# Optimization experiments

Hardware: AMD Instinct MI355X
Metric: run time of the kernel (lower is better)

The kernel has to match this reference:

```python
import jax, jax.numpy as jnp
import numpy as np

D, H, DH, L, F, NM = 512, 8, 64, 8, 2048, 80
B, S = 8, 1024


def _ln(x, g, b, eps=1e-5):
    mu = x.mean(-1, keepdims=True)
    var = ((x - mu) ** 2).mean(-1, keepdims=True)
    return (x - mu) / jnp.sqrt(var + eps) * g + b


def setup_inputs() -> dict:
    key = jax.random.key(0)
    ks = jax.random.split(key, 16)
    n = lambda k, sh: jax.random.normal(k, sh, dtype=jnp.float32) * 0.02
    # sinusoidal positional encoding, as in PositionalEncoding
    pos = np.arange(S, dtype=np.float32)[:, None]
    div = np.exp(np.arange(0, D, 2, dtype=np.float32) * (-np.log(10000.0) / D))
    pe = np.zeros((S, D), dtype=np.float32)
    pe[:, 0::2] = np.sin(pos * div)
    pe[:, 1::2] = np.cos(pos * div)
    return dict(
        mel=jax.random.normal(ks[0], (B, S, NM), dtype=jnp.float32),
        pe=jnp.asarray(pe),
        proj_w=n(ks[1], (NM, D)), proj_b=jnp.zeros((D,), jnp.float32),
        Wq=n(ks[2], (L, D, D)), bq=jnp.zeros((L, D), jnp.float32),
        Wk=n(ks[3], (L, D, D)), bk=jnp.zeros((L, D), jnp.float32),
        Wv=n(ks[4], (L, D, D)), bv=jnp.zeros((L, D), jnp.float32),
        Wo=n(ks[5], (L, D, D)), bo=jnp.zeros((L, D), jnp.float32),
        ln1_g=jnp.ones((L, D), jnp.float32), ln1_b=jnp.zeros((L, D), jnp.float32),
        ln2_g=jnp.ones((L, D), jnp.float32), ln2_b=jnp.zeros((L, D), jnp.float32),
        Wi=n(ks[6], (L, D, F)), bi=jnp.zeros((L, F), jnp.float32),
        Wf=n(ks[7], (L, F, D)), bf=jnp.zeros((L, D), jnp.float32),
        lnf_g=jnp.ones((D,), jnp.float32), lnf_b=jnp.zeros((D,), jnp.float32),
        lang_w=n(ks[8], (D, 100)), lang_b=jnp.zeros((100,), jnp.float32),
        int_w=n(ks[9], (D, 50)), int_b=jnp.zeros((50,), jnp.float32),
        emo_w=n(ks[10], (D, 8)), emo_b=jnp.zeros((8,), jnp.float32),
        sp_w=n(ks[11], (D, 1000)), sp_b=jnp.zeros((1000,), jnp.float32),
    )


def reference(mel, pe, proj_w, proj_b, Wq, bq, Wk, bk, Wv, bv, Wo, bo,
              ln1_g, ln1_b, ln2_g, ln2_b, Wi, bi, Wf, bf,
              lnf_g, lnf_b, lang_w, lang_b, int_w, int_b, emo_w, emo_b, sp_w, sp_b):
    # feature extraction projection + positional encoding
    h = mel @ proj_w + proj_b + pe[None]  # (B, S, D)
    scale = 1.0 / np.sqrt(DH)

    def block(h, p):
        wq, bq_, wk, bk_, wv, bv_, wo, bo_, g1, b1, g2, b2, wi, bi_, wf, bf_ = p
        x = _ln(h, g1, b1)
        b, s, _ = x.shape
        heads = lambda y, w, bias: (y @ w + bias).reshape(b, s, H, DH).transpose(0, 2, 1, 3)
        q, k, v = heads(x, wq, bq_), heads(x, wk, bk_), heads(x, wv, bv_)
        probs = jax.nn.softmax(jnp.einsum('bhqd,bhkd->bhqk', q, k) * scale, axis=-1)
        ctx = jnp.einsum('bhqk,bhkd->bhqd', probs, v).transpose(0, 2, 1, 3).reshape(b, s, D)
        h = h + ctx @ wo + bo_
        y = _ln(h, g2, b2)
        h = h + jax.nn.gelu(y @ wi + bi_, approximate=False) @ wf + bf_
        return h, None

    h, _ = jax.lax.scan(block, h, (Wq, bq, Wk, bk, Wv, bv, Wo, bo,
                                   ln1_g, ln1_b, ln2_g, ln2_b, Wi, bi, Wf, bf))
    h = _ln(h, lnf_g, lnf_b)
    pooled = h.mean(axis=1)  # no mask: sequence_lengths=None path
    language_logits = pooled @ lang_w + lang_b
    intent_logits = pooled @ int_w + int_b
    emotion_logits = pooled @ emo_w + emo_b
    speech_logits = h @ sp_w + sp_b
    return (language_logits, intent_logits, emotion_logits, speech_logits)
```

## Files before the change

### kernel.cpp

```cpp
#include <hip/hip_runtime.h>
#include <hip/hip_bf16.h>
#include <math.h>

#define DD   512
#define HH   8
#define DHH  64
#define LL   8
#define FF   2048
#define NMEL 80
#define BB   8
#define SS   1024
#define MM   (BB*SS)

typedef __attribute__((ext_vector_type(8))) short bf16x8;
typedef __attribute__((ext_vector_type(4))) float f32x4;
typedef __attribute__((ext_vector_type(4))) unsigned short u16x4;
typedef __attribute__((ext_vector_type(8))) unsigned short u16x8;

#define GLOAD_LDS16(g, l) __builtin_amdgcn_global_load_lds( \
    (const __attribute__((address_space(1))) void*)(g),      \
    (__attribute__((address_space(3))) void*)(l), 16, 0, 0)

__device__ __forceinline__ unsigned short f2bf(float x) {
    __hip_bfloat16 b = __float2bfloat16(x);
    return *reinterpret_cast<unsigned short*>(&b);
}

__global__ __launch_bounds__(256) void proj_pe_kernel(
    const float* __restrict__ mel, const float* __restrict__ pw,
    const float* __restrict__ pb, const float* __restrict__ pe,
    float* __restrict__ h)
{
    int row = blockIdx.x;
    int s = row & (SS - 1);
    __shared__ float m_s[NMEL];
    int t = threadIdx.x;
    if (t < NMEL) m_s[t] = mel[(size_t)row * NMEL + t];
    __syncthreads();
    for (int d = t; d < DD; d += 256) {
        float acc = pb[d] + pe[(size_t)s * DD + d];
        #pragma unroll 8
        for (int k = 0; k < NMEL; ++k)
            acc = fmaf(m_s[k], pw[(size_t)k * DD + d], acc);
        h[(size_t)row * DD + d] = acc;
    }
}

__global__ __launch_bounds__(512) void ln_kernel(
    const float* __restrict__ in, const float* __restrict__ g,
    const float* __restrict__ bta, __hip_bfloat16* __restrict__ out)
{
    int w = threadIdx.x >> 6, lane = threadIdx.x & 63;
    int row = blockIdx.x * 8 + w;
    const float4* xr = reinterpret_cast<const float4*>(in + (size_t)row * DD) + lane * 2;
    float4 v0 = xr[0], v1 = xr[1];
    float s  = v0.x + v0.y + v0.z + v0.w + v1.x + v1.y + v1.z + v1.w;
    float ss = v0.x*v0.x + v0.y*v0.y + v0.z*v0.z + v0.w*v0.w
             + v1.x*v1.x + v1.y*v1.y + v1.z*v1.z + v1.w*v1.w;
    #pragma unroll
    for (int off = 1; off < 64; off <<= 1) {
        s  += __shfl_xor(s, off);
        ss += __shfl_xor(ss, off);
    }
    float mu  = s * (1.f / DD);
    float var = ss * (1.f / DD) - mu * mu;
    float rstd = rsqrtf(var + 1e-5f);
    const float4* gp = reinterpret_cast<const float4*>(g) + lane * 2;
    const float4* bp = reinterpret_cast<const float4*>(bta) + lane * 2;
    float4 g0 = gp[0], g1 = gp[1], b0 = bp[0], b1 = bp[1];
    u16x8 o;
    o[0] = f2bf((v0.x - mu) * rstd * g0.x + b0.x);
    o[1] = f2bf((v0.y - mu) * rstd * g0.y + b0.y);
    o[2] = f2bf((v0.z - mu) * rstd * g0.z + b0.z);
    o[3] = f2bf((v0.w - mu) * rstd * g0.w + b0.w);
    o[4] = f2bf((v1.x - mu) * rstd * g1.x + b1.x);
    o[5] = f2bf((v1.y - mu) * rstd * g1.y + b1.y);
    o[6] = f2bf((v1.z - mu) * rstd * g1.z + b1.z);
    o[7] = f2bf((v1.w - mu) * rstd * g1.w + b1.w);
    *reinterpret_cast<u16x8*>(out + (size_t)row * DD + lane * 8) = o;
}

__global__ __launch_bounds__(256) void wconv_kernel(
    const float* __restrict__ in, __hip_bfloat16* __restrict__ out,
    int K, int N, int rstride, int rowoff)
{
    __shared__ float tile[32][33];
    size_t lin  = (size_t)blockIdx.z * K * N;
    size_t lout = (size_t)blockIdx.z * rstride * K + (size_t)rowoff * K;
    int tx = threadIdx.x & 31, ty = threadIdx.x >> 5;
    int n0 = blockIdx.x * 32, k0 = blockIdx.y * 32;
    #pragma unroll
    for (int i = 0; i < 32; i += 8) {
        int k = k0 + ty + i, n = n0 + tx;
        tile[ty + i][tx] = (n < N) ? in[lin + (size_t)k * N + n] : 0.f;
    }
    __syncthreads();
    #pragma unroll
    for (int i = 0; i < 32; i += 8) {
        int n = n0 + ty + i, k = k0 + tx;
        out[lout + (size_t)n * K + k] = __float2bfloat16(tile[tx][ty + i]);
    }
}

template<int OUTMODE, bool GELU_EP, bool RESID>
__global__ __launch_bounds__(512) void gemm_bf16(
    const __hip_bfloat16* __restrict__ A,
    const __hip_bfloat16* __restrict__ Bt,
    const float* __restrict__ b0, const float* __restrict__ b1,
    const float* __restrict__ b2,
    const float* __restrict__ resid,
    float* __restrict__ Cf,
    __hip_bfloat16* __restrict__ O0, __hip_bfloat16* __restrict__ O1,
    __hip_bfloat16* __restrict__ O2,
    int M, int N, int K)
{
    __shared__ __align__(16) __hip_bfloat16 As[128 * 64];
    __shared__ __align__(16) __hip_bfloat16 Bs[128 * 64];
    int t = threadIdx.x;
    int w = t >> 6, lane = t & 63, g = lane >> 4, li = lane & 15;
    int wm = w >> 2, wn = w & 3;

    int nwg = gridDim.x * gridDim.y;
    int lin = blockIdx.y * gridDim.x + blockIdx.x;
    int xcd = lin & 7, idx = lin >> 3;
    int q8 = nwg >> 3, r8 = nwg & 7;
    int swz = (xcd < r8 ? xcd * (q8 + 1) : r8 * (q8 + 1) + (xcd - r8) * q8) + idx;
    size_t bm = (size_t)(swz / gridDim.x) * 128;
    size_t bn = (size_t)(swz % gridDim.x) * 128;

    const f32x4 vzero = {0.f, 0.f, 0.f, 0.f};
    f32x4 acc[4][2];
    #pragma unroll
    for (int i = 0; i < 4; ++i)
        #pragma unroll
        for (int j = 0; j < 2; ++j) acc[i][j] = vzero;

    for (int k0 = 0; k0 < K; k0 += 64) {
        #pragma unroll
        for (int i = 0; i < 2; ++i) {
            int c = i * 512 + t;
            int row = c >> 3, col = (c & 7) << 3;
            GLOAD_LDS16(A + (bm + row) * (size_t)K + k0 + col, As + (size_t)c * 8);
        }
        #pragma unroll
        for (int i = 0; i < 2; ++i) {
            int c = i * 512 + t;
            int row = c >> 3, col = (c & 7) << 3;
            GLOAD_LDS16(Bt + (bn + row) * (size_t)K + k0 + col, Bs + (size_t)c * 8);
        }
        __syncthreads();
        #pragma unroll
        for (int kk = 0; kk < 2; ++kk) {
            bf16x8 af[4], bfr[2];
            #pragma unroll
            for (int mi = 0; mi < 4; ++mi)
                af[mi] = *reinterpret_cast<const bf16x8*>(As + (wm * 64 + mi * 16 + li) * 64 + kk * 32 + g * 8);
            #pragma unroll
            for (int ni = 0; ni < 2; ++ni)
                bfr[ni] = *reinterpret_cast<const bf16x8*>(Bs + (wn * 32 + ni * 16 + li) * 64 + kk * 32 + g * 8);
            #pragma unroll
            for (int mi = 0; mi < 4; ++mi)
                #pragma unroll
                for (int ni = 0; ni < 2; ++ni)
                    acc[mi][ni] = __builtin_amdgcn_mfma_f32_16x16x32_bf16(af[mi], bfr[ni], acc[mi][ni], 0, 0, 0);
        }
        __syncthreads();
    }

    #pragma unroll
    for (int mi = 0; mi < 4; ++mi) {
        #pragma unroll
        for (int ni = 0; ni < 2; ++ni) {
            f32x4 v = acc[mi][ni];
            int coll = wn * 32 + ni * 16 + li;
            size_t col = bn + coll;
            if ((int)col >= N) continue;
            float bv;
            int sel = 0, c = (int)col;
            if (OUTMODE == 2) {
                sel = (int)(col >> 9); c = (int)(col & 511);
                bv = (sel == 0) ? b0[c] : (sel == 1) ? b1[c] : b2[c];
            } else {
                bv = b0[col];
            }
            #pragma unroll
            for (int r = 0; r < 4; ++r) {
                size_t row = bm + wm * 64 + mi * 16 + g * 4 + r;
                float x = v[r] + bv;
                if (GELU_EP) x = 0.5f * x * (1.f + erff(x * 0.70710678118654752440f));
                if (RESID)   x += resid[row * (size_t)N + col];
                if (OUTMODE == 0) {
                    Cf[row * (size_t)N + col] = x;
                } else if (OUTMODE == 1) {
                    O0[row * (size_t)N + col] = __float2bfloat16(x);
                } else {
                    size_t b = row >> 10, s = row & (SS - 1);
                    size_t h = (size_t)(c >> 6), d = (size_t)(c & 63);
                    __hip_bfloat16 xb = __float2bfloat16(x);
                    if (sel == 0)      O0[((b * HH + h) << 16) + (s << 6) + d] = xb;
                    else if (sel == 1) O1[((b * HH + h) << 16) + (s << 6) + d] = xb;
                    else               O2[((b * HH + h) << 16) + (d << 10) + s] = xb;
                }
            }
        }
    }
}

__global__ __launch_bounds__(512, 4) void attn_mfma(
    const __hip_bfloat16* __restrict__ qb,
    const __hip_bfloat16* __restrict__ kb,
    const __hip_bfloat16* __restrict__ vtb,
    __hip_bfloat16* __restrict__ ctx)
{
    __shared__ __align__(16) char smem[49152];
    unsigned short (*Plds)[32][40] = (unsigned short (*)[32][40])smem;
    float* comb = (float*)smem;

    int t = threadIdx.x;
    int w = t >> 6, lane = t & 63, g = lane >> 4, li = lane & 15;
    int wq = w & 3, wk = w >> 2;
    int bh = blockIdx.x;
    int b = bh >> 3, h = bh & 7;
    int q0 = blockIdx.y * 128 + wq * 32;

    const __hip_bfloat16* Qp = qb  + ((size_t)bh << 16);
    const __hip_bfloat16* Kp = kb  + ((size_t)bh << 16);
    const __hip_bfloat16* Vp = vtb + ((size_t)bh << 16);

    bf16x8 qf[2][2];
    #pragma unroll
    for (int qt = 0; qt < 2; ++qt)
        #pragma unroll
        for (int kk = 0; kk < 2; ++kk)
            qf[qt][kk] = *reinterpret_cast<const bf16x8*>(
                Qp + (size_t)(q0 + qt * 16 + li) * DHH + kk * 32 + g * 8);

    const f32x4 vzero = {0.f, 0.f, 0.f, 0.f};
    f32x4 acc_oT[2][4];
    float m_r[2], l_r[2];
    #pragma unroll
    for (int qt = 0; qt < 2; ++qt) {
        #pragma unroll
        for (int dt = 0; dt < 4; ++dt) acc_oT[qt][dt] = vzero;
        m_r[qt] = -1e30f; l_r[qt] = 0.f;
    }

    const float csc = 0.125f * 1.44269504088896340736f;

    for (int it = 0; it < 16; ++it) {
        int ks0 = wk * 512 + it * 32;
        f32x4 accs[2][2];
        #pragma unroll
        for (int qt = 0; qt < 2; ++qt)
            #pragma unroll
            for (int kt = 0; kt < 2; ++kt) accs[qt][kt] = vzero;
        #pragma unroll
        for (int kk = 0; kk < 2; ++kk) {
            bf16x8 kf[2];
            #pragma unroll
            for (int kt = 0; kt < 2; ++kt)
                kf[kt] = *reinterpret_cast<const bf16x8*>(
                    Kp + (size_t)(ks0 + kt * 16 + li) * DHH + kk * 32 + g * 8);
            #pragma unroll
            for (int qt = 0; qt < 2; ++qt)
                #pragma unroll
                for (int kt = 0; kt < 2; ++kt)
                    accs[qt][kt] = __builtin_amdgcn_mfma_f32_16x16x32_bf16(kf[kt], qf[qt][kk], accs[qt][kt], 0, 0, 0);
        }

        float mnew[2];
        #pragma unroll
        for (int qt = 0; qt < 2; ++qt) {
            float a0 = fmaxf(fmaxf(accs[qt][0][0], accs[qt][0][1]),
                             fmaxf(accs[qt][0][2], accs[qt][0][3]));
            float a1 = fmaxf(fmaxf(accs[qt][1][0], accs[qt][1][1]),
                             fmaxf(accs[qt][1][2], accs[qt][1][3]));
            float m = fmaxf(a0, a1);
            m = fmaxf(m, __shfl_xor(m, 16));
            m = fmaxf(m, __shfl_xor(m, 32));
            mnew[qt] = m * csc;
        }

        bool grow = (mnew[0] > m_r[0] + 11.0f) || (mnew[1] > m_r[1] + 11.0f);
        if (__any(grow)) {
            #pragma unroll
            for (int qt = 0; qt < 2; ++qt) {
                float mn = fmaxf(m_r[qt], mnew[qt]);
                float alpha = exp2f(m_r[qt] - mn);
                m_r[qt] = mn;
                l_r[qt] *= alpha;
                #pragma unroll
                for (int dt = 0; dt < 4; ++dt)
                    #pragma unroll
                    for (int r = 0; r < 4; ++r)
                        acc_oT[qt][dt][r] *= alpha;
            }
        }

        float rs[2] = {0.f, 0.f};
        #pragma unroll
        for (int qt = 0; qt < 2; ++qt) {
            #pragma unroll
            for (int kt = 0; kt < 2; ++kt) {
                u16x4 pk;
                #pragma unroll
                for (int r = 0; r < 4; ++r) {
                    float p = exp2f(fmaf(accs[qt][kt][r], csc, -m_r[qt]));
                    rs[qt] += p;
                    pk[r] = f2bf(p);
                }
                *reinterpret_cast<u16x4*>(&Plds[w][qt * 16 + li][kt * 16 + g * 4]) = pk;
            }
            float s = rs[qt];
            s += __shfl_xor(s, 16);
            s += __shfl_xor(s, 32);
            l_r[qt] += s;
        }

        __builtin_amdgcn_wave_barrier();

        bf16x8 pf[2];
        #pragma unroll
        for (int qt = 0; qt < 2; ++qt)
            pf[qt] = *reinterpret_cast<const bf16x8*>(&Plds[w][qt * 16 + li][g * 8]);
        #pragma unroll
        for (int dt = 0; dt < 4; ++dt) {
            bf16x8 vf = *reinterpret_cast<const bf16x8*>(
                Vp + (size_t)(dt * 16 + li) * SS + ks0 + g * 8);
            #pragma unroll
            for (int qt = 0; qt < 2; ++qt)
                acc_oT[qt][dt] = __builtin_amdgcn_mfma_f32_16x16x32_bf16(vf, pf[qt], acc_oT[qt][dt], 0, 0, 0);
        }
        __builtin_amdgcn_wave_barrier();
    }

    __syncthreads();
    if (wk == 1) {
        float* cb = comb + ((size_t)(w - 4) * 64 + lane) * 36;
        #pragma unroll
        for (int qt = 0; qt < 2; ++qt)
            #pragma unroll
            for (int dt = 0; dt < 4; ++dt)
                *reinterpret_cast<f32x4*>(cb + qt * 16 + dt * 4) = acc_oT[qt][dt];
        #pragma unroll
        for (int qt = 0; qt < 2; ++qt) {
            cb[32 + qt] = m_r[qt];
            cb[34 + qt] = l_r[qt];
        }
    }
    __syncthreads();
    if (wk == 0) {
        float* cb = comb + ((size_t)w * 64 + lane) * 36;
        #pragma unroll
        for (int qt = 0; qt < 2; ++qt) {
            float m2 = cb[32 + qt];
            float l2 = cb[34 + qt];
            float mg = fmaxf(m_r[qt], m2);
            float a1 = exp2f(m_r[qt] - mg);
            float a2 = exp2f(m2 - mg);
            float inv = 1.f / (l_r[qt] * a1 + l2 * a2);
            int q = q0 + qt * 16 + li;
            #pragma unroll
            for (int dt = 0; dt < 4; ++dt) {
                f32x4 ob = *reinterpret_cast<const f32x4*>(cb + qt * 16 + dt * 4);
                u16x4 pk;
                #pragma unroll
                for (int r = 0; r < 4; ++r)
                    pk[r] = f2bf((acc_oT[qt][dt][r] * a1 + ob[r] * a2) * inv);
                *reinterpret_cast<u16x4*>(
                    &ctx[((size_t)(b * SS + q)) * DD + h * DHH + dt * 16 + g * 4]) = pk;
            }
        }
    }
}

__global__ __launch_bounds__(512) void pool_kernel(
    const __hip_bfloat16* __restrict__ hf, float* __restrict__ pooled)
{
    int b = blockIdx.x;
    int d = threadIdx.x;
    float acc = 0.f;
    for (int s = 0; s < SS; ++s)
        acc += __bfloat162float(hf[((size_t)(b * SS + s)) * DD + d]);
    pooled[b * DD + d] = acc * (1.f / SS);
}

__global__ __launch_bounds__(256) void heads_kernel(
    const float* __restrict__ pooled,
    const float* __restrict__ lw, const float* __restrict__ lb,
    const float* __restrict__ iw, const float* __restrict__ ib,
    const float* __restrict__ ew, const float* __restrict__ eb,
    float* __restrict__ out)
{
    int b = blockIdx.x;
    __shared__ float ps[DD];
    int t = threadIdx.x;
    ps[t] = pooled[b * DD + t];
    ps[t + 256] = pooled[b * DD + t + 256];
    __syncthreads();
    if (t < 158) {
        const float* wptr; const float* bptr; float* optr; int n; int j;
        if (t < 100)      { j = t;       wptr = lw; bptr = lb; optr = out;        n = 100; }
        else if (t < 150) { j = t - 100; wptr = iw; bptr = ib; optr = out + 800;  n = 50;  }
        else              { j = t - 150; wptr = ew; bptr = eb; optr = out + 1200; n = 8;   }
        float acc = bptr[j];
        for (int k2 = 0; k2 < DD; ++k2)
            acc = fmaf(ps[k2], wptr[(size_t)k2 * n + j], acc);
        optr[b * n + j] = acc;
    }
}

extern "C" void kernel_launch(void* const* d_in, const int* in_sizes, int n_in,
                              void* d_out, int out_size, void* d_ws, size_t ws_size,
                              hipStream_t stream)
{
    const float* mel    = (const float*)d_in[0];
    const float* pe     = (const float*)d_in[1];
    const float* proj_w = (const float*)d_in[2];
    const float* proj_b = (const float*)d_in[3];
    const float* Wq     = (const float*)d_in[4];
    const float* bq     = (const float*)d_in[5];
    const float* Wk     = (const float*)d_in[6];
    const float* bk     = (const float*)d_in[7];
    const float* Wv     = (const float*)d_in[8];
    const float* bv     = (const float*)d_in[9];
    const float* Wo     = (const float*)d_in[10];
    const float* bo     = (const float*)d_in[11];
    const float* ln1_g  = (const float*)d_in[12];
    const float* ln1_b  = (const float*)d_in[13];
    const float* ln2_g  = (const float*)d_in[14];
    const float* ln2_b  = (const float*)d_in[15];
    const float* Wi     = (const float*)d_in[16];
    const float* bi     = (const float*)d_in[17];
    const float* Wf     = (const float*)d_in[18];
    const float* bf     = (const float*)d_in[19];
    const float* lnf_g  = (const float*)d_in[20];
    const float* lnf_b  = (const float*)d_in[21];
    const float* lang_w = (const float*)d_in[22];
    const float* lang_b = (const float*)d_in[23];
    const float* int_w  = (const float*)d_in[24];
    const float* int_b  = (const float*)d_in[25];
    const float* emo_w  = (const float*)d_in[26];
    const float* emo_b  = (const float*)d_in[27];
    const float* sp_w   = (const float*)d_in[28];
    const float* sp_b   = (const float*)d_in[29];

    float* out = (float*)d_out;
    char* wsb = (char*)d_ws;

    const size_t MB = 1ull << 20;
    float* hbuf           = (float*)(wsb);
    __hip_bfloat16* xb    = (__hip_bfloat16*)(wsb + 16 * MB);
    __hip_bfloat16* qbuf  = (__hip_bfloat16*)(wsb + 24 * MB);
    __hip_bfloat16* kbuf  = (__hip_bfloat16*)(wsb + 32 * MB);
    __hip_bfloat16* vtb   = (__hip_bfloat16*)(wsb + 40 * MB);
    __hip_bfloat16* ctx   = (__hip_bfloat16*)(wsb + 48 * MB);
    __hip_bfloat16* gbuf  = (__hip_bfloat16*)(wsb + 24 * MB);
    float* pooled         = (float*)(wsb + 56 * MB);
    __hip_bfloat16* wqkv  = (__hip_bfloat16*)(wsb + 57 * MB);
    __hip_bfloat16* wot   = (__hip_bfloat16*)(wsb + 70 * MB);
    __hip_bfloat16* wit   = (__hip_bfloat16*)(wsb + 74 * MB);
    __hip_bfloat16* wft   = (__hip_bfloat16*)(wsb + 90 * MB);
    __hip_bfloat16* spt   = (__hip_bfloat16*)(wsb + 107 * MB);

    wconv_kernel<<<dim3(16, 16, LL), 256, 0, stream>>>(Wq, wqkv, DD, DD, 1536, 0);
    wconv_kernel<<<dim3(16, 16, LL), 256, 0, stream>>>(Wk, wqkv, DD, DD, 1536, 512);
    wconv_kernel<<<dim3(16, 16, LL), 256, 0, stream>>>(Wv, wqkv, DD, DD, 1536, 1024);
    wconv_kernel<<<dim3(16, 16, LL), 256, 0, stream>>>(Wo, wot, DD, DD, DD, 0);
    wconv_kernel<<<dim3(64, 16, LL), 256, 0, stream>>>(Wi, wit, DD, FF, FF, 0);
    wconv_kernel<<<dim3(16, 64, LL), 256, 0, stream>>>(Wf, wft, FF, DD, DD, 0);
    wconv_kernel<<<dim3(32, 16, 1),  256, 0, stream>>>(sp_w, spt, DD, 1000, 1024, 0);

    proj_pe_kernel<<<MM, 256, 0, stream>>>(mel, proj_w, proj_b, pe, hbuf);

    dim3 g512(4, 64);

    for (int l = 0; l < LL; ++l) {
        const __hip_bfloat16* wqkv_l = wqkv + (size_t)l * 1536 * DD;
        const __hip_bfloat16* wot_l  = wot  + (size_t)l * DD * DD;
        const __hip_bfloat16* wit_l  = wit  + (size_t)l * FF * DD;
        const __hip_bfloat16* wft_l  = wft  + (size_t)l * DD * FF;

        ln_kernel<<<MM / 8, 512, 0, stream>>>(hbuf, ln1_g + l * DD, ln1_b + l * DD, xb);

        gemm_bf16<2, false, false><<<dim3(12, 64), 512, 0, stream>>>(
            xb, wqkv_l, bq + l * DD, bk + l * DD, bv + l * DD,
            nullptr, nullptr, qbuf, kbuf, vtb, MM, 1536, DD);

        attn_mfma<<<dim3(BB * HH, SS / 128), 512, 0, stream>>>(qbuf, kbuf, vtb, ctx);

        gemm_bf16<0, false, true><<<g512, 512, 0, stream>>>(
            ctx, wot_l, bo + l * DD, nullptr, nullptr,
            hbuf, hbuf, nullptr, nullptr, nullptr, MM, DD, DD);

        ln_kernel<<<MM / 8, 512, 0, stream>>>(hbuf, ln2_g + l * DD, ln2_b + l * DD, xb);

        gemm_bf16<1, true, false><<<dim3(16, 64), 512, 0, stream>>>(
            xb, wit_l, bi + l * FF, nullptr, nullptr,
            nullptr, nullptr, gbuf, nullptr, nullptr, MM, FF, DD);
        gemm_bf16<0, false, true><<<g512, 512, 0, stream>>>(
            gbuf, wft_l, bf + l * DD, nullptr, nullptr,
            hbuf, hbuf, nullptr, nullptr, nullptr, MM, DD, FF);
    }

    ln_kernel<<<MM / 8, 512, 0, stream>>>(hbuf, lnf_g, lnf_b, xb);
    pool_kernel<<<BB, 512, 0, stream>>>(xb, pooled);
    heads_kernel<<<BB, 256, 0, stream>>>(pooled, lang_w, lang_b, int_w, int_b,
                                         emo_w, emo_b, out);

    gemm_bf16<0, false, false><<<dim3(8, 64), 512, 0, stream>>>(
        xb, spt, sp_b, nullptr, nullptr,
        nullptr, out + 1264, nullptr, nullptr, nullptr, MM, 1000, DD);
}
```

Measured before the change: 1.800 ms.

## Use 128x64 GEMM tiles for N=512 outputs, prefetch V in attention, split pooling

Adds a BN template parameter to the bf16 GEMM. The two N=512 residual GEMMs (Wo and Wf) now use 128x64 tiles, doubling their grid from 256 to 512 workgroups so more CUs have work. In attention, V fragments are loaded before the softmax instead of after it, the per-iteration wave barriers are removed, and the loop is unrolled by 2 to hide load latency. Pooling is split across 256 blocks that write partial sums, which the heads kernel then reduces. The smaller GEMM tiles cut per-wave MFMA work and reuse, and the earlier V loads raise register pressure.

```diff
diff --git a/kernel.cpp b/kernel.cpp
--- a/kernel.cpp
+++ b/kernel.cpp
@@ -102,7 +102,7 @@
     }
 }
 
-template<int OUTMODE, bool GELU_EP, bool RESID>
+template<int BN, int OUTMODE, bool GELU_EP, bool RESID>
 __global__ __launch_bounds__(512) void gemm_bf16(
     const __hip_bfloat16* __restrict__ A,
     const __hip_bfloat16* __restrict__ Bt,
@@ -114,26 +114,29 @@
     __hip_bfloat16* __restrict__ O2,
     int M, int N, int K)
 {
+    constexpr int MI = (BN == 128) ? 4 : 2;
+    constexpr int NI = 2;
     __shared__ __align__(16) __hip_bfloat16 As[128 * 64];
-    __shared__ __align__(16) __hip_bfloat16 Bs[128 * 64];
+    __shared__ __align__(16) __hip_bfloat16 Bs[BN * 64];
     int t = threadIdx.x;
     int w = t >> 6, lane = t & 63, g = lane >> 4, li = lane & 15;
-    int wm = w >> 2, wn = w & 3;
+    int wm = (BN == 128) ? (w >> 2) : (w >> 1);
+    int wn = (BN == 128) ? (w & 3) : (w & 1);
 
     int nwg = gridDim.x * gridDim.y;
-    int lin = blockIdx.y * gridDim.x + blockIdx.x;
-    int xcd = lin & 7, idx = lin >> 3;
+    int linb = blockIdx.y * gridDim.x + blockIdx.x;
+    int xcd = linb & 7, idx = linb >> 3;
     int q8 = nwg >> 3, r8 = nwg & 7;
     int swz = (xcd < r8 ? xcd * (q8 + 1) : r8 * (q8 + 1) + (xcd - r8) * q8) + idx;
     size_t bm = (size_t)(swz / gridDim.x) * 128;
-    size_t bn = (size_t)(swz % gridDim.x) * 128;
+    size_t bn = (size_t)(swz % gridDim.x) * BN;
 
     const f32x4 vzero = {0.f, 0.f, 0.f, 0.f};
-    f32x4 acc[4][2];
-    #pragma unroll
-    for (int i = 0; i < 4; ++i)
-        #pragma unroll
-        for (int j = 0; j < 2; ++j) acc[i][j] = vzero;
+    f32x4 acc[MI][NI];
+    #pragma unroll
+    for (int i = 0; i < MI; ++i)
+        #pragma unroll
+        for (int j = 0; j < NI; ++j) acc[i][j] = vzero;
 
     for (int k0 = 0; k0 < K; k0 += 64) {
         #pragma unroll
@@ -143,7 +146,7 @@
             GLOAD_LDS16(A + (bm + row) * (size_t)K + k0 + col, As + (size_t)c * 8);
         }
         #pragma unroll
-        for (int i = 0; i < 2; ++i) {
+        for (int i = 0; i < BN / 64; ++i) {
             int c = i * 512 + t;
             int row = c >> 3, col = (c & 7) << 3;
             GLOAD_LDS16(Bt + (bn + row) * (size_t)K + k0 + col, Bs + (size_t)c * 8);
@@ -151,26 +154,26 @@
         __syncthreads();
         #pragma unroll
         for (int kk = 0; kk < 2; ++kk) {
-            bf16x8 af[4], bfr[2];
-            #pragma unroll
-            for (int mi = 0; mi < 4; ++mi)
-                af[mi] = *reinterpret_cast<const bf16x8*>(As + (wm * 64 + mi * 16 + li) * 64 + kk * 32 + g * 8);
-            #pragma unroll
-            for (int ni = 0; ni < 2; ++ni)
+            bf16x8 af[MI], bfr[NI];
+            #pragma unroll
+            for (int mi = 0; mi < MI; ++mi)
+                af[mi] = *reinterpret_cast<const bf16x8*>(As + (wm * (MI * 16) + mi * 16 + li) * 64 + kk * 32 + g * 8);
+            #pragma unroll
+            for (int ni = 0; ni < NI; ++ni)
                 bfr[ni] = *reinterpret_cast<const bf16x8*>(Bs + (wn * 32 + ni * 16 + li) * 64 + kk * 32 + g * 8);
             #pragma unroll
-            for (int mi = 0; mi < 4; ++mi)
+            for (int mi = 0; mi < MI; ++mi)
                 #pragma unroll
-                for (int ni = 0; ni < 2; ++ni)
+                for (int ni = 0; ni < NI; ++ni)
                     acc[mi][ni] = __builtin_amdgcn_mfma_f32_16x16x32_bf16(af[mi], bfr[ni], acc[mi][ni], 0, 0, 0);
         }
         __syncthreads();
     }
 
     #pragma unroll
-    for (int mi = 0; mi < 4; ++mi) {
-        #pragma unroll
-        for (int ni = 0; ni < 2; ++ni) {
+    for (int mi = 0; mi < MI; ++mi) {
+        #pragma unroll
+        for (int ni = 0; ni < NI; ++ni) {
             f32x4 v = acc[mi][ni];
             int coll = wn * 32 + ni * 16 + li;
             size_t col = bn + coll;
@@ -185,7 +188,7 @@
             }
             #pragma unroll
             for (int r = 0; r < 4; ++r) {
-                size_t row = bm + wm * 64 + mi * 16 + g * 4 + r;
+                size_t row = bm + wm * (MI * 16) + mi * 16 + g * 4 + r;
                 float x = v[r] + bv;
                 if (GELU_EP) x = 0.5f * x * (1.f + erff(x * 0.70710678118654752440f));
                 if (RESID)   x += resid[row * (size_t)N + col];
@@ -247,6 +250,7 @@
 
     const float csc = 0.125f * 1.44269504088896340736f;
 
+    #pragma unroll 2
     for (int it = 0; it < 16; ++it) {
         int ks0 = wk * 512 + it * 32;
         f32x4 accs[2][2];
@@ -267,6 +271,12 @@
                 for (int kt = 0; kt < 2; ++kt)
                     accs[qt][kt] = __builtin_amdgcn_mfma_f32_16x16x32_bf16(kf[kt], qf[qt][kk], accs[qt][kt], 0, 0, 0);
         }
+
+        bf16x8 vf[4];
+        #pragma unroll
+        for (int dt = 0; dt < 4; ++dt)
+            vf[dt] = *reinterpret_cast<const bf16x8*>(
+                Vp + (size_t)(dt * 16 + li) * SS + ks0 + g * 8);
 
         float mnew[2];
         #pragma unroll
@@ -317,21 +327,15 @@
             l_r[qt] += s;
         }
 
-        __builtin_amdgcn_wave_barrier();
-
         bf16x8 pf[2];
         #pragma unroll
         for (int qt = 0; qt < 2; ++qt)
             pf[qt] = *reinterpret_cast<const bf16x8*>(&Plds[w][qt * 16 + li][g * 8]);
         #pragma unroll
-        for (int dt = 0; dt < 4; ++dt) {
-            bf16x8 vf = *reinterpret_cast<const bf16x8*>(
-                Vp + (size_t)(dt * 16 + li) * SS + ks0 + g * 8);
+        for (int dt = 0; dt < 4; ++dt)
             #pragma unroll
             for (int qt = 0; qt < 2; ++qt)
-                acc_oT[qt][dt] = __builtin_amdgcn_mfma_f32_16x16x32_bf16(vf, pf[qt], acc_oT[qt][dt], 0, 0, 0);
-        }
-        __builtin_amdgcn_wave_barrier();
+                acc_oT[qt][dt] = __builtin_amdgcn_mfma_f32_16x16x32_bf16(vf[dt], pf[qt], acc_oT[qt][dt], 0, 0, 0);
     }
 
     __syncthreads();
@@ -375,18 +379,19 @@
 }
 
 __global__ __launch_bounds__(512) void pool_kernel(
-    const __hip_bfloat16* __restrict__ hf, float* __restrict__ pooled)
-{
-    int b = blockIdx.x;
+    const __hip_bfloat16* __restrict__ hf, float* __restrict__ part)
+{
+    int b = blockIdx.x >> 5, chunk = blockIdx.x & 31;
     int d = threadIdx.x;
     float acc = 0.f;
-    for (int s = 0; s < SS; ++s)
+    int s0 = chunk * 32;
+    for (int s = s0; s < s0 + 32; ++s)
         acc += __bfloat162float(hf[((size_t)(b * SS + s)) * DD + d]);
-    pooled[b * DD + d] = acc * (1.f / SS);
+    part[(size_t)blockIdx.x * DD + d] = acc;
 }
 
 __global__ __launch_bounds__(256) void heads_kernel(
-    const float* __restrict__ pooled,
+    const float* __restrict__ part,
     const float* __restrict__ lw, const float* __restrict__ lb,
     const float* __restrict__ iw, const float* __restrict__ ib,
     const float* __restrict__ ew, const float* __restrict__ eb,
@@ -395,8 +400,14 @@
     int b = blockIdx.x;
     __shared__ float ps[DD];
     int t = threadIdx.x;
-    ps[t] = pooled[b * DD + t];
-    ps[t + 256] = pooled[b * DD + t + 256];
+    float a0 = 0.f, a1 = 0.f;
+    for (int c = 0; c < 32; ++c) {
+        const float* p = part + ((size_t)(b * 32 + c)) * DD;
+        a0 += p[t];
+        a1 += p[t + 256];
+    }
+    ps[t]       = a0 * (1.f / SS);
+    ps[t + 256] = a1 * (1.f / SS);
     __syncthreads();
     if (t < 158) {
         const float* wptr; const float* bptr; float* optr; int n; int j;
@@ -456,7 +467,7 @@
     __hip_bfloat16* vtb   = (__hip_bfloat16*)(wsb + 40 * MB);
     __hip_bfloat16* ctx   = (__hip_bfloat16*)(wsb + 48 * MB);
     __hip_bfloat16* gbuf  = (__hip_bfloat16*)(wsb + 24 * MB);
-    float* pooled         = (float*)(wsb + 56 * MB);
+    float* part           = (float*)(wsb + 56 * MB);
     __hip_bfloat16* wqkv  = (__hip_bfloat16*)(wsb + 57 * MB);
     __hip_bfloat16* wot   = (__hip_bfloat16*)(wsb + 70 * MB);
     __hip_bfloat16* wit   = (__hip_bfloat16*)(wsb + 74 * MB);
@@ -473,8 +484,6 @@
 
     proj_pe_kernel<<<MM, 256, 0, stream>>>(mel, proj_w, proj_b, pe, hbuf);
 
-    dim3 g512(4, 64);
-
     for (int l = 0; l < LL; ++l) {
         const __hip_bfloat16* wqkv_l = wqkv + (size_t)l * 1536 * DD;
         const __hip_bfloat16* wot_l  = wot  + (size_t)l * DD * DD;
@@ -483,32 +492,32 @@
 
         ln_kernel<<<MM / 8, 512, 0, stream>>>(hbuf, ln1_g + l * DD, ln1_b + l * DD, xb);
 
-        gemm_bf16<2, false, false><<<dim3(12, 64), 512, 0, stream>>>(
+        gemm_bf16<128, 2, false, false><<<dim3(12, 64), 512, 0, stream>>>(
             xb, wqkv_l, bq + l * DD, bk + l * DD, bv + l * DD,
             nullptr, nullptr, qbuf, kbuf, vtb, MM, 1536, DD);
 
         attn_mfma<<<dim3(BB * HH, SS / 128), 512, 0, stream>>>(qbuf, kbuf, vtb, ctx);
 
-        gemm_bf16<0, false, true><<<g512, 512, 0, stream>>>(
+        gemm_bf16<64, 0, false, true><<<dim3(8, 64), 512, 0, stream>>>(
             ctx, wot_l, bo + l * DD, nullptr, nullptr,
             hbuf, hbuf, nullptr, nullptr, nullptr, MM, DD, DD);
 
         ln_kernel<<<MM / 8, 512, 0, stream>>>(hbuf, ln2_g + l * DD, ln2_b + l * DD, xb);
 
-        gemm_bf16<1, true, false><<<dim3(16, 64), 512, 0, stream>>>(
+        gemm_bf16<128, 1, true, false><<<dim3(16, 64), 512, 0, stream>>>(
             xb, wit_l, bi + l * FF, nullptr, nullptr,
             nullptr, nullptr, gbuf, nullptr, nullptr, MM, FF, DD);
-        gemm_bf16<0, false, true><<<g512, 512, 0, stream>>>(
+        gemm_bf16<64, 0, false, true><<<dim3(8, 64), 512, 0, stream>>>(
             gbuf, wft_l, bf + l * DD, nullptr, nullptr,
             hbuf, hbuf, nullptr, nullptr, nullptr, MM, DD, FF);
     }
 
     ln_kernel<<<MM / 8, 512, 0, stream>>>(hbuf, lnf_g, lnf_b, xb);
-    pool_kernel<<<BB, 512, 0, stream>>>(xb, pooled);
-    heads_kernel<<<BB, 256, 0, stream>>>(pooled, lang_w, lang_b, int_w, int_b,
+    pool_kernel<<<BB * 32, 512, 0, stream>>>(xb, part);
+    heads_kernel<<<BB, 256, 0, stream>>>(part, lang_w, lang_b, int_w, int_b,
                                          emo_w, emo_b, out);
 
-    gemm_bf16<0, false, false><<<dim3(8, 64), 512, 0, stream>>>(
+    gemm_bf16<128, 0, false, false><<<dim3(8, 64), 512, 0, stream>>>(
         xb, spt, sp_b, nullptr, nullptr,
         nullptr, out + 1264, nullptr, nullptr, nullptr, MM, 1000, DD);
 }
```

Result: faster. 1.701 ms, median of 2 (-5.5%).
